# Kernel optimization log

Hardware: AMD Instinct MI355X
Metric: run time of the kernel (lower is better)

The kernel has to match this reference:

```python
import jax, jax.numpy as jnp
import numpy as np

CP_DIMS = (8, 8)      # control-point grid (matches init cp_dims)
EPS = 1e-10           # epsilon used by tf interpolate_spline _phi


def ndgrid(dims):
    """Normalized (y, x) grid, shape [prod(dims), 2], values in [0, 1]."""
    g = np.mgrid[:dims[0], :dims[1]].reshape(2, -1).T.astype(np.float32)
    g = g / (np.array(dims, dtype=np.float32) - 1.0)
    return jnp.asarray(g)


def _phi(r2):
    # order-2 TPS kernel on SQUARED distances: 0.5 * r2 * log(max(r2, eps))
    return 0.5 * r2 * jnp.log(jnp.maximum(r2, EPS))


def _sq_dist(a, b):
    # a: [m, d], b: [n, d] -> [m, n] squared distances
    d = a[:, None, :] - b[None, :, :]
    return jnp.sum(d * d, axis=-1)


def setup_inputs() -> dict:
    key = jax.random.key(0)
    k1, k2 = jax.random.split(key)
    vol = jax.random.normal(k1, (16, 256, 256, 16), dtype=jnp.float32)
    # small offsets in normalized [0,1] coordinates
    cp_offsets = jax.random.normal(k2, (16, 64, 2), dtype=jnp.float32) * 0.05
    return {"vol": vol, "cp_offsets": cp_offsets}


def reference(vol, cp_offsets):
    B, H, W, C = vol.shape
    cp = ndgrid(CP_DIMS)          # [n, 2] train points (fixed, inverse=False)
    q = ndgrid((H, W))            # [m, 2] query points
    n = cp.shape[0]
    m = q.shape[0]

    # ---- TPS solve (train points fixed across batch -> single LHS) ----
    A = _phi(_sq_dist(cp, cp))                              # [n, n]
    Bmat = jnp.concatenate([cp, jnp.ones((n, 1), cp.dtype)], axis=1)  # [n, 3]
    top = jnp.concatenate([A, Bmat], axis=1)                # [n, n+3]
    bot = jnp.concatenate([Bmat.T, jnp.zeros((3, 3), cp.dtype)], axis=1)
    lhs = jnp.concatenate([top, bot], axis=0)               # [n+3, n+3]

    warped = cp[None, :, :] + cp_offsets                    # [B, n, 2] train values
    rhs = jnp.concatenate([warped, jnp.zeros((B, 3, 2), vol.dtype)], axis=1)
    wv = jnp.linalg.solve(lhs[None], rhs)                   # [B, n+3, 2]
    w, v = wv[:, :n, :], wv[:, n:, :]                       # [B,n,2], [B,3,2]

    # ---- TPS apply at all pixel locations ----
    phi_q = _phi(_sq_dist(q, cp))                           # [m, n]
    q_aug = jnp.concatenate([q, jnp.ones((m, 1), q.dtype)], axis=1)  # [m, 3]
    loc = jnp.einsum('mn,bnk->bmk', phi_q, w) + jnp.einsum('mp,bpk->bmk', q_aug, v)
    # loc is (y, x) normalized; reverse -> (x, y) then scale to pixels
    x = loc[..., 1] * (W - 1)                               # [B, m]
    y = loc[..., 0] * (H - 1)

    # ---- bilinear resampling with zero padding (tf resampler semantics) ----
    x0 = jnp.floor(x); y0 = jnp.floor(y)
    wx = x - x0; wy = y - y0
    x0i = x0.astype(jnp.int32); y0i = y0.astype(jnp.int32)
    x1i = x0i + 1; y1i = y0i + 1

    vol_flat = vol.reshape(B, H * W, C)

    def gather(yi, xi):
        valid = (yi >= 0) & (yi < H) & (xi >= 0) & (xi < W)
        idx = jnp.clip(yi, 0, H - 1) * W + jnp.clip(xi, 0, W - 1)  # [B, m]
        vals = jnp.take_along_axis(vol_flat, idx[..., None], axis=1)  # [B, m, C]
        return vals * valid[..., None].astype(vol.dtype)

    out = (gather(y0i, x0i) * ((1 - wy) * (1 - wx))[..., None]
           + gather(y0i, x1i) * ((1 - wy) * wx)[..., None]
           + gather(y1i, x0i) * (wy * (1 - wx))[..., None]
           + gather(y1i, x1i) * (wy * wx)[..., None])
    return out.reshape(B, H, W, C)
```

## Files before the change

kernel.cpp:

```cpp
#include <hip/hip_runtime.h>
#include <math.h>
#include <string.h>

#define HH 256
#define WW 256
#define CC 16
#define BB 16
#define NCP 64
#define NA 67

typedef float f32x4 __attribute__((ext_vector_type(4)));

static void build_M(float* Mf , float* wv0 )
{
    static double A[NA][NA + NCP];
    for (int r = 0; r < NA; ++r) {
        for (int c = 0; c < NA; ++c) {
            double val;
            if (r < NCP && c < NCP) {
                double ry = (double)(r >> 3) / 7.0, rx = (double)(r & 7) / 7.0;
                double cy = (double)(c >> 3) / 7.0, cx = (double)(c & 7) / 7.0;
                double dy = ry - cy, dx = rx - cx;
                double r2 = dy * dy + dx * dx;
                val = 0.5 * r2 * log(r2 > 1e-10 ? r2 : 1e-10);
            } else if (r < NCP) {
                int k = c - NCP;
                val = (k == 0) ? (double)(r >> 3) / 7.0
                    : (k == 1) ? (double)(r & 7) / 7.0 : 1.0;
            } else if (c < NCP) {
                int k = r - NCP;
                val = (k == 0) ? (double)(c >> 3) / 7.0
                    : (k == 1) ? (double)(c & 7) / 7.0 : 1.0;
            } else {
                val = 0.0;
            }
            A[r][c] = val;
        }
        for (int c = 0; c < NCP; ++c) A[r][NA + c] = (r == c) ? 1.0 : 0.0;
    }
    for (int p = 0; p < NA; ++p) {
        int best = p; double bv = fabs(A[p][p]);
        for (int r = p + 1; r < NA; ++r) {
            double v = fabs(A[r][p]);
            if (v > bv) { bv = v; best = r; }
        }
        if (best != p)
            for (int j = 0; j < NA + NCP; ++j) {
                double t = A[p][j]; A[p][j] = A[best][j]; A[best][j] = t;
            }
        double ip = 1.0 / A[p][p];
        for (int j = 0; j < NA + NCP; ++j) A[p][j] *= ip;
        for (int r = 0; r < NA; ++r) {
            if (r == p) continue;
            double f = A[r][p];
            if (f != 0.0)
                for (int j = 0; j < NA + NCP; ++j) A[r][j] -= f * A[p][j];
        }
    }
    for (int r = 0; r < NA; ++r) {
        double s0 = 0.0, s1 = 0.0;
        for (int n = 0; n < NCP; ++n) {
            double m = A[r][NA + n];
            Mf[r * NCP + n] = (float)m;
            s0 += m * ((double)(n >> 3) / 7.0);
            s1 += m * ((double)(n & 7) / 7.0);
        }
        wv0[r * 2 + 0] = (float)s0;
        wv0[r * 2 + 1] = (float)s1;
    }
}

struct ConstBlob { float M[NA * NCP]; float wv0[NA * 2]; };

__global__ __launch_bounds__(256) void tps_coef_kernel(
    ConstBlob cb, const float* __restrict__ cp_offsets, float* __restrict__ wv)
{
    const int b = blockIdx.x;
    const int t = threadIdx.x;
    __shared__ float sOff[NCP * 2];
    if (t < NCP * 2) sOff[t] = cp_offsets[b * NCP * 2 + t];
    __syncthreads();
    if (t >= NA * 2) return;
    const int k = t & 1;
    const int r = t >> 1;
    float s = cb.wv0[r * 2 + k];
    const float* Mr = cb.M + r * NCP;
#pragma unroll
    for (int n = 0; n < NCP; ++n) s += Mr[n] * sOff[n * 2 + k];
    const float scale = (r < NCP) ? (255.0f * 0.5f * 0.69314718055994531f) : 255.0f;
    wv[(b * 2 + k) * NA + r] = s * scale;
}

__global__ __launch_bounds__(256) void tps_warp_kernel(
    const float* __restrict__ vol, const float* __restrict__ wv,
    float* __restrict__ out)
{
    const int id = blockIdx.x;
    const int xcd = id & 7;
    const int j = id >> 3;
    const int b = (xcd << 1) | (j >> 8);
    const int y = j & 255;
    const int x = threadIdx.x;

    __shared__ int4   sI[WW];
    __shared__ float4 sW[WW];

    const float* __restrict__ wY = wv + (size_t)b * 2 * NA;
    const float* __restrict__ wX = wY + NA;

    const float qy = (float)y * (1.0f / 255.0f);
    const float qx = (float)x * (1.0f / 255.0f);
    float fy = qy * wY[NCP] + qx * wY[NCP + 1] + wY[NCP + 2];
    float fx = qy * wX[NCP] + qx * wX[NCP + 1] + wX[NCP + 2];

    float dy2[8], dx2[8];
#pragma unroll
    for (int i = 0; i < 8; ++i) {
        float dy = qy - (float)i * (1.0f / 7.0f);
        float dx = qx - (float)i * (1.0f / 7.0f);
        dy2[i] = dy * dy;
        dx2[i] = dx * dx;
    }
#pragma unroll
    for (int i = 0; i < 8; ++i) {
        const float s_ = dy2[i];
#pragma unroll
        for (int jj = 0; jj < 8; ++jj) {
            const int n = i * 8 + jj;
            float r2 = s_ + dx2[jj];
            float t_ = __log2f(fmaxf(r2, 1e-10f));
            float p = r2 * t_;
            fy += p * wY[n];
            fx += p * wX[n];
        }
    }

    float x0f = floorf(fx), y0f = floorf(fy);
    float wxf = fx - x0f, wyf = fy - y0f;
    int x0 = (int)x0f, y0 = (int)y0f;
    int x1 = x0 + 1, y1 = y0 + 1;
    bool vx0 = (x0 >= 0) && (x0 < WW), vx1 = (x1 >= 0) && (x1 < WW);
    bool vy0 = (y0 >= 0) && (y0 < HH), vy1 = (y1 >= 0) && (y1 < HH);
    int x0c = min(max(x0, 0), WW - 1), x1c = min(max(x1, 0), WW - 1);
    int y0c = min(max(y0, 0), HH - 1), y1c = min(max(y1, 0), HH - 1);
    float4 w4;
    w4.x = (1.f - wyf) * (1.f - wxf) * ((vy0 && vx0) ? 1.f : 0.f);
    w4.y = (1.f - wyf) * wxf         * ((vy0 && vx1) ? 1.f : 0.f);
    w4.z = wyf * (1.f - wxf)         * ((vy1 && vx0) ? 1.f : 0.f);
    w4.w = wyf * wxf                 * ((vy1 && vx1) ? 1.f : 0.f);
    sW[x] = w4;
    sI[x] = make_int4((y0c * WW + x0c) * 4, (y0c * WW + x1c) * 4,
                      (y1c * WW + x0c) * 4, (y1c * WW + x1c) * 4);
    __syncthreads();

    const float4* __restrict__ vb =
        (const float4*)vol + (size_t)b * (HH * WW * (CC / 4));
    f32x4* __restrict__ ob =
        (f32x4*)out + ((size_t)b * HH * WW + (size_t)y * WW) * (CC / 4);
    const int cq = x & 3;
#pragma unroll
    for (int k = 0; k < 4; ++k) {
        const int p = (x >> 2) + 64 * k;
        int4   I = sI[p];
        float4 Wt = sW[p];
        float4 a  = vb[I.x + cq];
        float4 bq = vb[I.y + cq];
        float4 c_ = vb[I.z + cq];
        float4 d_ = vb[I.w + cq];
        f32x4 r;
        r.x = a.x * Wt.x + bq.x * Wt.y + c_.x * Wt.z + d_.x * Wt.w;
        r.y = a.y * Wt.x + bq.y * Wt.y + c_.y * Wt.z + d_.y * Wt.w;
        r.z = a.z * Wt.x + bq.z * Wt.y + c_.z * Wt.z + d_.z * Wt.w;
        r.w = a.w * Wt.x + bq.w * Wt.y + c_.w * Wt.z + d_.w * Wt.w;
        __builtin_nontemporal_store(r, &ob[x + 256 * k]);
    }
}

extern "C" void kernel_launch(void* const* d_in, const int* in_sizes, int n_in,
                              void* d_out, int out_size, void* d_ws, size_t ws_size,
                              hipStream_t stream)
{
    const float* vol = (const float*)d_in[0];
    const float* cpo = (const float*)d_in[1];
    float* out = (float*)d_out;
    float* d_wv = (float*)d_ws;

    static ConstBlob cb;
    build_M(cb.M, cb.wv0);

    tps_coef_kernel<<<dim3(BB), dim3(256), 0, stream>>>(cb, cpo, d_wv);
    tps_warp_kernel<<<dim3(HH * BB), dim3(256), 0, stream>>>(vol, d_wv, out);
}
```

Before: 125.9 us.

## Split TPS evaluation and bilinear gather across 4-lane quads with DPP reductions

Each output pixel is now handled by a quad of four lanes. Each lane evaluates 16 of the 64 TPS kernel terms and the partial sums are combined with DPP quad reductions. Each lane then fetches one bilinear corner's 16 channels, weights it, and quad-reduces, which removes the shared-memory staging and the block barrier. The coefficients are padded to a stride of 68 so they can be loaded as float4 vectors, the grid grows fourfold, and the nontemporal store is replaced by a plain store. The trade-off is many extra DPP shuffles per pixel (32 for the channel reduction alone) and a select to pick the output channel group.

```diff
diff --git a/kernel.cpp b/kernel.cpp
--- a/kernel.cpp
+++ b/kernel.cpp
@@ -8,6 +8,7 @@
 #define BB 16
 #define NCP 64
 #define NA 67
+#define WVS 68
 
 typedef float f32x4 __attribute__((ext_vector_type(4)));
 
@@ -80,15 +81,26 @@
     __shared__ float sOff[NCP * 2];
     if (t < NCP * 2) sOff[t] = cp_offsets[b * NCP * 2 + t];
     __syncthreads();
-    if (t >= NA * 2) return;
-    const int k = t & 1;
-    const int r = t >> 1;
-    float s = cb.wv0[r * 2 + k];
-    const float* Mr = cb.M + r * NCP;
-#pragma unroll
-    for (int n = 0; n < NCP; ++n) s += Mr[n] * sOff[n * 2 + k];
-    const float scale = (r < NCP) ? (255.0f * 0.5f * 0.69314718055994531f) : 255.0f;
-    wv[(b * 2 + k) * NA + r] = s * scale;
+    if (t < NA * 2) {
+        const int k = t & 1;
+        const int r = t >> 1;
+        float s = cb.wv0[r * 2 + k];
+        const float* Mr = cb.M + r * NCP;
+#pragma unroll
+        for (int n = 0; n < NCP; ++n) s += Mr[n] * sOff[n * 2 + k];
+        const float scale = (r < NCP) ? (255.0f * 0.5f * 0.69314718055994531f) : 255.0f;
+        wv[(b * 2 + k) * WVS + r] = s * scale;
+    } else if (t < NA * 2 + 2) {
+        wv[(b * 2 + (t - NA * 2)) * WVS + 67] = 0.0f;
+    }
+}
+
+__device__ __forceinline__ float quad_sum(float v)
+{
+    int v1 = __builtin_amdgcn_update_dpp(0, __float_as_int(v), 0xB1, 0xF, 0xF, true);
+    float s = v + __int_as_float(v1);
+    int v2 = __builtin_amdgcn_update_dpp(0, __float_as_int(s), 0x4E, 0xF, 0xF, true);
+    return s + __int_as_float(v2);
 }
 
 __global__ __launch_bounds__(256) void tps_warp_kernel(
@@ -98,82 +110,85 @@
     const int id = blockIdx.x;
     const int xcd = id & 7;
     const int j = id >> 3;
-    const int b = (xcd << 1) | (j >> 8);
-    const int y = j & 255;
-    const int x = threadIdx.x;
-
-    __shared__ int4   sI[WW];
-    __shared__ float4 sW[WW];
-
-    const float* __restrict__ wY = wv + (size_t)b * 2 * NA;
-    const float* __restrict__ wX = wY + NA;
+    const int b = (xcd << 1) | (j >> 10);
+    const int rr = j & 1023;
+    const int y = rr >> 2;
+    const int xseg = rr & 3;
+    const int tid = threadIdx.x;
+    const int cq = tid & 3;
+    const int px = (xseg << 6) + (tid >> 2);
+
+    const f32x4* __restrict__ w4 = (const f32x4*)(wv + (size_t)b * 2 * WVS);
+    const int wo = cq << 2;
+    const f32x4 wY0 = w4[wo + 0], wY1 = w4[wo + 1], wY2 = w4[wo + 2], wY3 = w4[wo + 3];
+    const f32x4 wX0 = w4[17 + wo], wX1 = w4[17 + wo + 1], wX2 = w4[17 + wo + 2], wX3 = w4[17 + wo + 3];
+    const f32x4 aY = w4[16];
+    const f32x4 aX = w4[33];
 
     const float qy = (float)y * (1.0f / 255.0f);
-    const float qx = (float)x * (1.0f / 255.0f);
-    float fy = qy * wY[NCP] + qx * wY[NCP + 1] + wY[NCP + 2];
-    float fx = qy * wX[NCP] + qx * wX[NCP + 1] + wX[NCP + 2];
-
-    float dy2[8], dx2[8];
-#pragma unroll
-    for (int i = 0; i < 8; ++i) {
-        float dy = qy - (float)i * (1.0f / 7.0f);
-        float dx = qx - (float)i * (1.0f / 7.0f);
-        dy2[i] = dy * dy;
-        dx2[i] = dx * dx;
-    }
-#pragma unroll
-    for (int i = 0; i < 8; ++i) {
-        const float s_ = dy2[i];
-#pragma unroll
-        for (int jj = 0; jj < 8; ++jj) {
-            const int n = i * 8 + jj;
-            float r2 = s_ + dx2[jj];
-            float t_ = __log2f(fmaxf(r2, 1e-10f));
-            float p = r2 * t_;
-            fy += p * wY[n];
-            fx += p * wX[n];
-        }
-    }
+    const float qx = (float)px * (1.0f / 255.0f);
+
+    float dx2[8];
+#pragma unroll
+    for (int c = 0; c < 8; ++c) {
+        float dx = qx - (float)c * (1.0f / 7.0f);
+        dx2[c] = dx * dx;
+    }
+    const float dy0 = qy - (float)(2 * cq) * (1.0f / 7.0f);
+    const float dy1 = qy - (float)(2 * cq + 1) * (1.0f / 7.0f);
+    const float dy20 = dy0 * dy0, dy21 = dy1 * dy1;
+
+    float fy = 0.f, fx = 0.f;
+#pragma unroll
+    for (int c = 0; c < 8; ++c) {
+        float r2 = dy20 + dx2[c];
+        float p = r2 * __log2f(fmaxf(r2, 1e-10f));
+        float wy_ = (c < 4) ? wY0[c] : wY1[c - 4];
+        float wx_ = (c < 4) ? wX0[c] : wX1[c - 4];
+        fy += p * wy_;
+        fx += p * wx_;
+    }
+#pragma unroll
+    for (int c = 0; c < 8; ++c) {
+        float r2 = dy21 + dx2[c];
+        float p = r2 * __log2f(fmaxf(r2, 1e-10f));
+        float wy_ = (c < 4) ? wY2[c] : wY3[c - 4];
+        float wx_ = (c < 4) ? wX2[c] : wX3[c - 4];
+        fy += p * wy_;
+        fx += p * wx_;
+    }
+    fy = quad_sum(fy);
+    fx = quad_sum(fx);
+    fy += qy * aY.x + qx * aY.y + aY.z;
+    fx += qy * aX.x + qx * aX.y + aX.z;
 
     float x0f = floorf(fx), y0f = floorf(fy);
     float wxf = fx - x0f, wyf = fy - y0f;
     int x0 = (int)x0f, y0 = (int)y0f;
     int x1 = x0 + 1, y1 = y0 + 1;
-    bool vx0 = (x0 >= 0) && (x0 < WW), vx1 = (x1 >= 0) && (x1 < WW);
-    bool vy0 = (y0 >= 0) && (y0 < HH), vy1 = (y1 >= 0) && (y1 < HH);
-    int x0c = min(max(x0, 0), WW - 1), x1c = min(max(x1, 0), WW - 1);
-    int y0c = min(max(y0, 0), HH - 1), y1c = min(max(y1, 0), HH - 1);
-    float4 w4;
-    w4.x = (1.f - wyf) * (1.f - wxf) * ((vy0 && vx0) ? 1.f : 0.f);
-    w4.y = (1.f - wyf) * wxf         * ((vy0 && vx1) ? 1.f : 0.f);
-    w4.z = wyf * (1.f - wxf)         * ((vy1 && vx0) ? 1.f : 0.f);
-    w4.w = wyf * wxf                 * ((vy1 && vx1) ? 1.f : 0.f);
-    sW[x] = w4;
-    sI[x] = make_int4((y0c * WW + x0c) * 4, (y0c * WW + x1c) * 4,
-                      (y1c * WW + x0c) * 4, (y1c * WW + x1c) * 4);
-    __syncthreads();
-
-    const float4* __restrict__ vb =
-        (const float4*)vol + (size_t)b * (HH * WW * (CC / 4));
-    f32x4* __restrict__ ob =
-        (f32x4*)out + ((size_t)b * HH * WW + (size_t)y * WW) * (CC / 4);
-    const int cq = x & 3;
-#pragma unroll
-    for (int k = 0; k < 4; ++k) {
-        const int p = (x >> 2) + 64 * k;
-        int4   I = sI[p];
-        float4 Wt = sW[p];
-        float4 a  = vb[I.x + cq];
-        float4 bq = vb[I.y + cq];
-        float4 c_ = vb[I.z + cq];
-        float4 d_ = vb[I.w + cq];
-        f32x4 r;
-        r.x = a.x * Wt.x + bq.x * Wt.y + c_.x * Wt.z + d_.x * Wt.w;
-        r.y = a.y * Wt.x + bq.y * Wt.y + c_.y * Wt.z + d_.y * Wt.w;
-        r.z = a.z * Wt.x + bq.z * Wt.y + c_.z * Wt.z + d_.z * Wt.w;
-        r.w = a.w * Wt.x + bq.w * Wt.y + c_.w * Wt.z + d_.w * Wt.w;
-        __builtin_nontemporal_store(r, &ob[x + 256 * k]);
-    }
+    int cx_ = (cq & 1) ? x1 : x0;
+    int cy_ = (cq & 2) ? y1 : y0;
+    bool valid = (cx_ >= 0) && (cx_ < WW) && (cy_ >= 0) && (cy_ < HH);
+    int cxc = min(max(cx_, 0), WW - 1);
+    int cyc = min(max(cy_, 0), HH - 1);
+    float wc = ((cq & 1) ? wxf : 1.f - wxf) * ((cq & 2) ? wyf : 1.f - wyf)
+             * (valid ? 1.f : 0.f);
+
+    const f32x4* __restrict__ vp = (const f32x4*)vol
+        + ((size_t)b * (HH * WW) + (size_t)(cyc * WW + cxc)) * (CC / 4);
+    f32x4 a0 = vp[0] * wc, a1 = vp[1] * wc, a2 = vp[2] * wc, a3 = vp[3] * wc;
+#pragma unroll
+    for (int c = 0; c < 4; ++c) {
+        a0[c] = quad_sum(a0[c]);
+        a1[c] = quad_sum(a1[c]);
+        a2[c] = quad_sum(a2[c]);
+        a3[c] = quad_sum(a3[c]);
+    }
+    f32x4 o = (cq == 0) ? a0 : (cq == 1) ? a1 : (cq == 2) ? a2 : a3;
+
+    f32x4* __restrict__ ob = (f32x4*)out
+        + ((size_t)b * (HH * WW) + (size_t)y * WW) * (CC / 4);
+    ob[(px << 2) + cq] = o;
 }
 
 extern "C" void kernel_launch(void* const* d_in, const int* in_sizes, int n_in,
@@ -189,5 +204,5 @@
     build_M(cb.M, cb.wv0);
 
     tps_coef_kernel<<<dim3(BB), dim3(256), 0, stream>>>(cb, cpo, d_wv);
-    tps_warp_kernel<<<dim3(HH * BB), dim3(256), 0, stream>>>(vol, d_wv, out);
-}
+    tps_warp_kernel<<<dim3(HH * BB * 4), dim3(256), 0, stream>>>(vol, d_wv, out);
+}
```

Result: slower. 145.5 us (+15.6%).
